# Performance work log

Hardware: AMD Instinct MI355X
Metric: run time of the kernel (lower is better)

The kernel has to match this reference:

```python
import jax, jax.numpy as jnp
import numpy as np

D_MODEL = 1024
N_HEADS = 16
D_HEAD = D_MODEL // N_HEADS
ROPE_BASE = 10000.0


def setup_inputs() -> dict:
    key = jax.random.key(0)
    k1, k2, k3, k4, k5 = jax.random.split(key, 5)
    std = 0.02 / np.sqrt(2 * 12)  # scaled_xavier with n_layers=12
    x = jax.random.normal(k1, (2, 2048, D_MODEL), dtype=jnp.float32)
    qkv_w = jax.random.normal(k2, (3 * D_MODEL, D_MODEL), dtype=jnp.float32) * std
    qkv_b = jnp.zeros((3 * D_MODEL,), dtype=jnp.float32)
    proj_w = jax.random.normal(k3, (D_MODEL, D_MODEL), dtype=jnp.float32) * std
    proj_b = jnp.zeros((D_MODEL,), dtype=jnp.float32)
    return {"x": x, "qkv_w": qkv_w, "qkv_b": qkv_b, "proj_w": proj_w, "proj_b": proj_b}


def _rope_cos_sin(seq_len, dtype):
    inv_freq = 1.0 / (ROPE_BASE ** (jnp.arange(0, D_HEAD, 2, dtype=jnp.float32) / D_HEAD))
    t = jnp.arange(seq_len, dtype=jnp.float32)
    freqs = jnp.einsum("t,d->td", t, inv_freq)          # [S, Dh/2]
    freqs = jnp.concatenate([freqs, freqs], axis=-1)      # [S, Dh]
    return jnp.cos(freqs).astype(dtype), jnp.sin(freqs).astype(dtype)


def _rotate_half(x):
    x1, x2 = jnp.split(x, 2, axis=-1)
    return jnp.concatenate([-x2, x1], axis=-1)


def reference(x, qkv_w, qkv_b, proj_w, proj_b):
    B, S, D = x.shape
    H, Dh = N_HEADS, D_HEAD
    scale = 1.0 / np.sqrt(Dh)

    qkv = x @ qkv_w.T + qkv_b                              # [B, S, 3D]
    qkv = qkv.reshape(B, S, 3, H, Dh)
    q = jnp.transpose(qkv[:, :, 0], (0, 2, 1, 3))          # [B, H, S, Dh]
    k = jnp.transpose(qkv[:, :, 1], (0, 2, 1, 3))
    v = jnp.transpose(qkv[:, :, 2], (0, 2, 1, 3))

    cos, sin = _rope_cos_sin(S, x.dtype)                   # [S, Dh]
    q = q * cos + _rotate_half(q) * sin
    k = k * cos + _rotate_half(k) * sin

    scores = jnp.einsum("bhsd,bhtd->bhst", q, k) * scale   # [B, H, S, S]
    causal = jnp.triu(jnp.ones((S, S), dtype=bool), k=1)
    neg = jnp.finfo(scores.dtype).min
    scores = jnp.where(causal[None, None], neg, scores)

    probs = jax.nn.softmax(scores, axis=-1)
    ctx = jnp.einsum("bhst,bhtd->bhsd", probs, v)          # [B, H, S, Dh]
    out = jnp.transpose(ctx, (0, 2, 1, 3)).reshape(B, S, D)
    out = out @ proj_w.T + proj_b
    return out
```

## Files before the change

### kernel.cpp

```cpp
#include <hip/hip_runtime.h>
#include <hip/hip_bf16.h>

#define BATCH 2
#define SEQ   2048
#define DMODEL 1024
#define NHEADS 16
#define DHEAD  64
#define MTOT   (BATCH * SEQ)
#define QKSTR  2048

typedef __attribute__((ext_vector_type(8))) short bf16x8;
typedef __attribute__((ext_vector_type(4))) float f32x4;

__device__ __forceinline__ void glds16(const void* g, void* l)
{
    __builtin_amdgcn_global_load_lds(
        (const __attribute__((address_space(1))) unsigned int*)g,
        (__attribute__((address_space(3))) unsigned int*)l, 16, 0, 0);
}

__global__ void cast_all_kernel(
    const float* __restrict__ a, __hip_bfloat16* __restrict__ oa, int na4,
    const float* __restrict__ b, __hip_bfloat16* __restrict__ ob, int nb4,
    const float* __restrict__ c, __hip_bfloat16* __restrict__ oc, int nc4)
{
    int i = blockIdx.x * blockDim.x + threadIdx.x;
    const float* src; __hip_bfloat16* dst; int j = i;
    if (j < na4) { src = a; dst = oa; }
    else {
        j -= na4;
        if (j < nb4) { src = b; dst = ob; }
        else {
            j -= nb4;
            if (j >= nc4) return;
            src = c; dst = oc;
        }
    }
    float4 v = ((const float4*)src)[j];
    __hip_bfloat16 tmp[4];
    tmp[0] = __float2bfloat16(v.x);
    tmp[1] = __float2bfloat16(v.y);
    tmp[2] = __float2bfloat16(v.z);
    tmp[3] = __float2bfloat16(v.w);
    *(uint2*)(dst + 4 * (size_t)j) = *(const uint2*)tmp;
}

#define GTM 64
#define GBK 64

__device__ __forceinline__ void store_out(float* p, float v) { *p = v; }
__device__ __forceinline__ void store_out(__hip_bfloat16* p, float v) { *p = __float2bfloat16(v); }

template <typename OutT, int MODE, int TN>
__global__ __launch_bounds__(256, 6) void gemm_bias_kernel(
    const __hip_bfloat16* __restrict__ A, const __hip_bfloat16* __restrict__ W,
    const float* __restrict__ bias, OutT* __restrict__ out,
    __hip_bfloat16* __restrict__ vtg,
    int M, int N, int K)
{
    const int NI = TN / 32;
    const int bm = blockIdx.x * GTM;
    const int bn = blockIdx.y * TN;
    const int tid = threadIdx.x;
    const int wave = tid >> 6;
    const int lane = tid & 63;
    const int quad = lane >> 4;
    const int l16 = lane & 15;
    const int wm = (wave & 1) * 32;
    const int wn = (wave >> 1) * (TN / 2);

    __shared__ __hip_bfloat16 As[GTM * GBK];
    __shared__ __hip_bfloat16 Bs[TN * GBK];

    f32x4 acc[2][NI] = {};

    const int srow = lane >> 3;
    const int gc8 = (((lane & 7) ^ srow)) * 8;

    for (int kt = 0; kt < K; kt += GBK) {
#pragma unroll
        for (int t = 0; t < 2; t++) {
            int i = wave * 2 + t;
            glds16(A + (size_t)(bm + i * 8 + srow) * K + kt + gc8, As + i * 512);
        }
#pragma unroll
        for (int t = 0; t < TN / 32; t++) {
            int i = wave * (TN / 32) + t;
            glds16(W + (size_t)(bn + i * 8 + srow) * K + kt + gc8, Bs + i * 512);
        }
        __syncthreads();

#pragma unroll
        for (int kk = 0; kk < 2; kk++) {
            bf16x8 af[2], bfr[NI];
#pragma unroll
            for (int i = 0; i < 2; i++) {
                int ra = wm + i * 16 + l16;
                af[i] = *(const bf16x8*)(As + ra * 64 + (((kk << 2) + quad) ^ (ra & 7)) * 8);
            }
#pragma unroll
            for (int i = 0; i < NI; i++) {
                int rb = wn + i * 16 + l16;
                bfr[i] = *(const bf16x8*)(Bs + rb * 64 + (((kk << 2) + quad) ^ (rb & 7)) * 8);
            }
#pragma unroll
            for (int mi = 0; mi < 2; mi++)
#pragma unroll
                for (int ni = 0; ni < NI; ni++)
                    acc[mi][ni] = __builtin_amdgcn_mfma_f32_16x16x32_bf16(
                        af[mi], bfr[ni], acc[mi][ni], 0, 0, 0);
        }
        __syncthreads();
    }

    if (MODE == 1 && (bn + wn) < 2 * DMODEL) {
#pragma unroll
        for (int ni = 0; ni < 2; ni++) {
            int col = bn + wn + ni * 16 + l16;
            int i32 = col & 31;
            float invf = exp2f(-13.287712379549449f * (float)i32 * (1.0f / 32.0f));
            float b1 = bias[col], b2 = bias[col + 32];
#pragma unroll
            for (int mi = 0; mi < 2; mi++) {
#pragma unroll
                for (int r = 0; r < 4; r++) {
                    int row = bm + wm + mi * 16 + quad * 4 + r;
                    int s = row & (SEQ - 1);
                    float ang = (float)s * invf;
                    float sn, cs;
                    __sincosf(ang, &sn, &cs);
                    float x1 = acc[mi][ni][r] + b1;
                    float x2 = acc[mi][ni + 2][r] + b2;
                    store_out(&out[(size_t)row * QKSTR + col], x1 * cs - x2 * sn);
                    store_out(&out[(size_t)row * QKSTR + col + 32], x2 * cs + x1 * sn);
                }
            }
        }
    } else if (MODE == 1) {
#pragma unroll
        for (int ni = 0; ni < NI; ni++) {
            int colg = bn + wn + ni * 16 + l16;
            int vcol = colg - 2 * DMODEL;
            int hh = vcol >> 6, dh = vcol & 63;
            float bv = bias[colg];
#pragma unroll
            for (int mi = 0; mi < 2; mi++) {
                int row0 = bm + wm + mi * 16 + quad * 4;
                int bb = row0 >> 11;
                int ss = row0 & (SEQ - 1);
                __hip_bfloat16 tmp[4];
#pragma unroll
                for (int r = 0; r < 4; r++)
                    tmp[r] = __float2bfloat16(acc[mi][ni][r] + bv);
                *(uint2*)(vtg + (((size_t)bb * NHEADS + hh) * DHEAD + dh) * SEQ + ss) =
                    *(uint2*)tmp;
            }
        }
    } else {
#pragma unroll
        for (int mi = 0; mi < 2; mi++)
#pragma unroll
            for (int ni = 0; ni < NI; ni++) {
                int col = bn + wn + ni * 16 + l16;
                float bv = bias[col];
#pragma unroll
                for (int r = 0; r < 4; r++) {
                    int row = bm + wm + mi * 16 + quad * 4 + r;
                    store_out(&out[(size_t)row * N + col], acc[mi][ni][r] + bv);
                }
            }
    }
}

__global__ __launch_bounds__(512, 4) void flash_attn_mfma_kernel(
    const __hip_bfloat16* __restrict__ qkb,
    const __hip_bfloat16* __restrict__ vtg,
    __hip_bfloat16* __restrict__ ctx)
{
    const int bh = blockIdx.x;
    const int b = bh >> 4, h = bh & 15;
    const int y = blockIdx.y;
    const int qa = y, qb = 31 - y;
    const int tid = threadIdx.x;
    const int w = tid >> 6;
    const int lane = tid & 63;
    const int quad = lane >> 4;
    const int l16 = lane & 15;
    const int w4 = w & 3;
    const int qt = (w >> 2) ? qb : qa;

    __shared__ __hip_bfloat16 Ks[2][64 * 64];
    __shared__ __hip_bfloat16 Vt[2][64 * 64];
    __shared__ __hip_bfloat16 Ps[128 * 64];

    const __hip_bfloat16* qbase = qkb + (size_t)b * SEQ * QKSTR + h * DHEAD;
    const __hip_bfloat16* kbase = qbase + DMODEL;
    const __hip_bfloat16* vbase = vtg + (size_t)bh * DHEAD * SEQ;

    const __hip_bfloat16* qrow = qbase + (size_t)(qt * 64 + w4 * 16 + l16) * QKSTR;
    bf16x8 qf0 = *(const bf16x8*)(qrow + quad * 8);
    bf16x8 qf1 = *(const bf16x8*)(qrow + 32 + quad * 8);

    const int srow = lane >> 3;
    const int gc8 = ((lane & 7) ^ srow) * 8;
    const __hip_bfloat16* kg = kbase + (size_t)(w * 8 + srow) * QKSTR + gc8;
    const __hip_bfloat16* vg = vbase + (size_t)(w * 8 + srow) * SEQ + gc8;

    const int xr = l16 & 7;
    const int fo0 = l16 * 64 + ((quad ^ xr) << 3);
    const int fo1 = l16 * 64 + (((4 + quad) ^ xr) << 3);
    const int pband = w * 16;
    const int pfo0 = (pband + l16) * 64 + ((quad ^ xr) << 3);
    const int pfo1 = (pband + l16) * 64 + (((4 + quad) ^ xr) << 3);

    const short onev = (l16 == 0) ? (short)0x3F80 : (short)0;
    const bf16x8 ones = {onev, onev, onev, onev, onev, onev, onev, onev};

    glds16(kg, &Ks[0][w * 512]);
    glds16(vg, &Vt[0][w * 512]);

    f32x4 oacc[5] = {};

    for (int jt = 0; jt <= qb; jt++) {
        __syncthreads();
        const int cur = jt & 1;
        if (jt < qb) {
            glds16(kg + (size_t)(jt + 1) * 64 * QKSTR, &Ks[cur ^ 1][w * 512]);
            glds16(vg + (jt + 1) * 64, &Vt[cur ^ 1][w * 512]);
        }
        if (jt <= qt) {
            const __hip_bfloat16* ks = Ks[cur];
            const __hip_bfloat16* vs = Vt[cur];

            f32x4 s4[4] = {};
#pragma unroll
            for (int nt = 0; nt < 4; nt++)
                s4[nt] = __builtin_amdgcn_mfma_f32_16x16x32_bf16(
                    qf0, *(const bf16x8*)(ks + nt * 1024 + fo0), s4[nt], 0, 0, 0);
#pragma unroll
            for (int nt = 0; nt < 4; nt++)
                s4[nt] = __builtin_amdgcn_mfma_f32_16x16x32_bf16(
                    qf1, *(const bf16x8*)(ks + nt * 1024 + fo1), s4[nt], 0, 0, 0);

            const bool diag = (jt == qt);
#pragma unroll
            for (int nt = 0; nt < 4; nt++)
#pragma unroll
                for (int r = 0; r < 4; r++) {
                    float p = __expf(s4[nt][r] * 0.125f);
                    if (diag)
                        p = (nt * 16 + l16 <= w4 * 16 + quad * 4 + r) ? p : 0.f;
                    int rr = quad * 4 + r;
                    Ps[(pband + rr) * 64 +
                       (((nt * 2 + (l16 >> 3)) ^ (rr & 7)) << 3) + xr] =
                        __float2bfloat16(p);
                }

            bf16x8 pf0 = *(const bf16x8*)(Ps + pfo0);
            bf16x8 pf1 = *(const bf16x8*)(Ps + pfo1);
#pragma unroll
            for (int dt = 0; dt < 4; dt++)
                oacc[dt] = __builtin_amdgcn_mfma_f32_16x16x32_bf16(
                    pf0, *(const bf16x8*)(vs + dt * 1024 + fo0), oacc[dt], 0, 0, 0);
            oacc[4] = __builtin_amdgcn_mfma_f32_16x16x32_bf16(pf0, ones, oacc[4], 0, 0, 0);
#pragma unroll
            for (int dt = 0; dt < 4; dt++)
                oacc[dt] = __builtin_amdgcn_mfma_f32_16x16x32_bf16(
                    pf1, *(const bf16x8*)(vs + dt * 1024 + fo1), oacc[dt], 0, 0, 0);
            oacc[4] = __builtin_amdgcn_mfma_f32_16x16x32_bf16(pf1, ones, oacc[4], 0, 0, 0);
        }
    }

#pragma unroll
    for (int r = 0; r < 4; r++) {
        float lv = __shfl(oacc[4][r], lane & 48);
        float il = 1.0f / lv;
        int qg = qt * 64 + w4 * 16 + quad * 4 + r;
        __hip_bfloat16* op = ctx + (((size_t)b * SEQ + qg) * NHEADS + h) * DHEAD + l16;
#pragma unroll
        for (int dt = 0; dt < 4; dt++)
            op[dt * 16] = __float2bfloat16(oacc[dt][r] * il);
    }
}

extern "C" void kernel_launch(void* const* d_in, const int* in_sizes, int n_in,
                              void* d_out, int out_size, void* d_ws, size_t ws_size,
                              hipStream_t stream)
{
    const float* x      = (const float*)d_in[0];
    const float* qkv_w  = (const float*)d_in[1];
    const float* qkv_b  = (const float*)d_in[2];
    const float* proj_w = (const float*)d_in[3];
    const float* proj_b = (const float*)d_in[4];
    float* out = (float*)d_out;

    char* w = (char*)d_ws;
    __hip_bfloat16* qkb = (__hip_bfloat16*)w;  w += (size_t)MTOT * QKSTR * 2;
    __hip_bfloat16* vtg = (__hip_bfloat16*)w;  w += (size_t)MTOT * DMODEL * 2;
    __hip_bfloat16* ctx = (__hip_bfloat16*)w;  w += (size_t)MTOT * DMODEL * 2;
    __hip_bfloat16* xb  = (__hip_bfloat16*)w;  w += (size_t)MTOT * DMODEL * 2;
    __hip_bfloat16* wqk = (__hip_bfloat16*)w;  w += (size_t)3 * DMODEL * DMODEL * 2;
    __hip_bfloat16* wpr = (__hip_bfloat16*)w;

    const int na4 = MTOT * DMODEL / 4;
    const int nb4 = 3 * DMODEL * DMODEL / 4;
    const int nc4 = DMODEL * DMODEL / 4;

    cast_all_kernel<<<(na4 + nb4 + nc4 + 255) / 256, 256, 0, stream>>>(
        x, xb, na4, qkv_w, wqk, nb4, proj_w, wpr, nc4);

    gemm_bias_kernel<__hip_bfloat16, 1, 128>
        <<<dim3(MTOT / GTM, (3 * DMODEL) / 128), 256, 0, stream>>>(
        xb, wqk, qkv_b, qkb, vtg, MTOT, 3 * DMODEL, DMODEL);

    flash_attn_mfma_kernel<<<dim3(BATCH * NHEADS, 16), 512, 0, stream>>>(qkb, vtg, ctx);

    gemm_bias_kernel<float, 0, 64>
        <<<dim3(MTOT / GTM, DMODEL / 64), 256, 0, stream>>>(
        ctx, wpr, proj_b, out, nullptr, MTOT, DMODEL, DMODEL);
}
```

Before: 175.1 us.

## Split long causal tile across both wave groups after short tile completes

After the short query tile finishes, the wave group that handled it now takes alternate KV tiles for the long query tile instead of idling. Partial numerator and denominator accumulators are then summed through shared memory before the output is written. K/V staging becomes a 4-slot ring that loads two tiles per iteration, and exp uses exp2 with a folded log2e scale. This raises LDS use and register pressure, which may reduce occupancy.

After: 175.3 us. About the same (+0.1%).

```diff
diff --git a/kernel.cpp b/kernel.cpp
--- a/kernel.cpp
+++ b/kernel.cpp
@@ -187,19 +187,23 @@
     const int quad = lane >> 4;
     const int l16 = lane & 15;
     const int w4 = w & 3;
-    const int qt = (w >> 2) ? qb : qa;
-
-    __shared__ __hip_bfloat16 Ks[2][64 * 64];
-    __shared__ __hip_bfloat16 Vt[2][64 * 64];
-    __shared__ __hip_bfloat16 Ps[128 * 64];
+    const int grp = w >> 2;
+    const int qtp = grp ? qb : qa;
+
+    __shared__ alignas(16) __hip_bfloat16 Ks[4][64 * 64];
+    __shared__ alignas(16) __hip_bfloat16 Vt[4][64 * 64];
+    __shared__ alignas(16) __hip_bfloat16 Ps[128 * 64];
 
     const __hip_bfloat16* qbase = qkb + (size_t)b * SEQ * QKSTR + h * DHEAD;
     const __hip_bfloat16* kbase = qbase + DMODEL;
     const __hip_bfloat16* vbase = vtg + (size_t)bh * DHEAD * SEQ;
 
-    const __hip_bfloat16* qrow = qbase + (size_t)(qt * 64 + w4 * 16 + l16) * QKSTR;
-    bf16x8 qf0 = *(const bf16x8*)(qrow + quad * 8);
-    bf16x8 qf1 = *(const bf16x8*)(qrow + 32 + quad * 8);
+    const __hip_bfloat16* qrowp = qbase + (size_t)(qtp * 64 + w4 * 16 + l16) * QKSTR;
+    bf16x8 qp0 = *(const bf16x8*)(qrowp + quad * 8);
+    bf16x8 qp1 = *(const bf16x8*)(qrowp + 32 + quad * 8);
+    const __hip_bfloat16* qrows = qbase + (size_t)(qb * 64 + w4 * 16 + l16) * QKSTR;
+    bf16x8 qs0 = *(const bf16x8*)(qrows + quad * 8);
+    bf16x8 qs1 = *(const bf16x8*)(qrows + 32 + quad * 8);
 
     const int srow = lane >> 3;
     const int gc8 = ((lane & 7) ^ srow) * 8;
@@ -216,70 +220,103 @@
     const short onev = (l16 == 0) ? (short)0x3F80 : (short)0;
     const bf16x8 ones = {onev, onev, onev, onev, onev, onev, onev, onev};
 
-    glds16(kg, &Ks[0][w * 512]);
-    glds16(vg, &Vt[0][w * 512]);
-
     f32x4 oacc[5] = {};
-
-    for (int jt = 0; jt <= qb; jt++) {
+    f32x4 oacc2[5] = {};
+
+    auto stage = [&](int t) {
+        glds16(kg + (size_t)t * 64 * QKSTR, &Ks[t & 3][w * 512]);
+        glds16(vg + t * 64, &Vt[t & 3][w * 512]);
+    };
+
+    auto compute = [&](const __hip_bfloat16* ks, const __hip_bfloat16* vs,
+                       bf16x8 f0, bf16x8 f1, f32x4* oa, bool diag) {
+        f32x4 s4[4] = {};
+#pragma unroll
+        for (int nt = 0; nt < 4; nt++)
+            s4[nt] = __builtin_amdgcn_mfma_f32_16x16x32_bf16(
+                f0, *(const bf16x8*)(ks + nt * 1024 + fo0), s4[nt], 0, 0, 0);
+#pragma unroll
+        for (int nt = 0; nt < 4; nt++)
+            s4[nt] = __builtin_amdgcn_mfma_f32_16x16x32_bf16(
+                f1, *(const bf16x8*)(ks + nt * 1024 + fo1), s4[nt], 0, 0, 0);
+
+#pragma unroll
+        for (int nt = 0; nt < 4; nt++)
+#pragma unroll
+            for (int r = 0; r < 4; r++) {
+                float p = exp2f(s4[nt][r] * 0.1803368801f);
+                if (diag)
+                    p = (nt * 16 + l16 <= w4 * 16 + quad * 4 + r) ? p : 0.f;
+                int rr = quad * 4 + r;
+                Ps[(pband + rr) * 64 +
+                   (((nt * 2 + (l16 >> 3)) ^ (rr & 7)) << 3) + xr] =
+                    __float2bfloat16(p);
+            }
+
+        bf16x8 pf0 = *(const bf16x8*)(Ps + pfo0);
+        bf16x8 pf1 = *(const bf16x8*)(Ps + pfo1);
+#pragma unroll
+        for (int dt = 0; dt < 4; dt++)
+            oa[dt] = __builtin_amdgcn_mfma_f32_16x16x32_bf16(
+                pf0, *(const bf16x8*)(vs + dt * 1024 + fo0), oa[dt], 0, 0, 0);
+        oa[4] = __builtin_amdgcn_mfma_f32_16x16x32_bf16(pf0, ones, oa[4], 0, 0, 0);
+#pragma unroll
+        for (int dt = 0; dt < 4; dt++)
+            oa[dt] = __builtin_amdgcn_mfma_f32_16x16x32_bf16(
+                pf1, *(const bf16x8*)(vs + dt * 1024 + fo1), oa[dt], 0, 0, 0);
+        oa[4] = __builtin_amdgcn_mfma_f32_16x16x32_bf16(pf1, ones, oa[4], 0, 0, 0);
+    };
+
+    stage(0);
+    const int nit = qa + 1 + ((qb - qa + 1) >> 1);
+
+    for (int n = 0; n < nit; n++) {
         __syncthreads();
-        const int cur = jt & 1;
-        if (jt < qb) {
-            glds16(kg + (size_t)(jt + 1) * 64 * QKSTR, &Ks[cur ^ 1][w * 512]);
-            glds16(vg + (jt + 1) * 64, &Vt[cur ^ 1][w * 512]);
-        }
-        if (jt <= qt) {
-            const __hip_bfloat16* ks = Ks[cur];
-            const __hip_bfloat16* vs = Vt[cur];
-
-            f32x4 s4[4] = {};
-#pragma unroll
-            for (int nt = 0; nt < 4; nt++)
-                s4[nt] = __builtin_amdgcn_mfma_f32_16x16x32_bf16(
-                    qf0, *(const bf16x8*)(ks + nt * 1024 + fo0), s4[nt], 0, 0, 0);
-#pragma unroll
-            for (int nt = 0; nt < 4; nt++)
-                s4[nt] = __builtin_amdgcn_mfma_f32_16x16x32_bf16(
-                    qf1, *(const bf16x8*)(ks + nt * 1024 + fo1), s4[nt], 0, 0, 0);
-
-            const bool diag = (jt == qt);
-#pragma unroll
-            for (int nt = 0; nt < 4; nt++)
-#pragma unroll
-                for (int r = 0; r < 4; r++) {
-                    float p = __expf(s4[nt][r] * 0.125f);
-                    if (diag)
-                        p = (nt * 16 + l16 <= w4 * 16 + quad * 4 + r) ? p : 0.f;
-                    int rr = quad * 4 + r;
-                    Ps[(pband + rr) * 64 +
-                       (((nt * 2 + (l16 >> 3)) ^ (rr & 7)) << 3) + xr] =
-                        __float2bfloat16(p);
-                }
-
-            bf16x8 pf0 = *(const bf16x8*)(Ps + pfo0);
-            bf16x8 pf1 = *(const bf16x8*)(Ps + pfo1);
+        if (n < qa) {
+            stage(n + 1);
+        } else {
+            int t0n = 2 * n - qa + 1;
+            if (t0n <= qb) stage(t0n);
+            if (t0n + 1 <= qb) stage(t0n + 1);
+        }
+        if (n <= qa) {
+            compute(&Ks[n & 3][0], &Vt[n & 3][0], qp0, qp1, oacc, n == qtp);
+        } else {
+            int t = 2 * n - qa - 1 + grp;
+            if (t <= qb) {
+                if (grp) compute(&Ks[t & 3][0], &Vt[t & 3][0], qp0, qp1, oacc, t == qb);
+                else     compute(&Ks[t & 3][0], &Vt[t & 3][0], qs0, qs1, oacc2, t == qb);
+            }
+        }
+    }
+
+    auto write_ctx = [&](f32x4* oa, int qt) {
+#pragma unroll
+        for (int r = 0; r < 4; r++) {
+            float lv = __shfl(oa[4][r], lane & 48);
+            float il = 1.0f / lv;
+            int qg = qt * 64 + w4 * 16 + quad * 4 + r;
+            __hip_bfloat16* op = ctx + (((size_t)b * SEQ + qg) * NHEADS + h) * DHEAD + l16;
 #pragma unroll
             for (int dt = 0; dt < 4; dt++)
-                oacc[dt] = __builtin_amdgcn_mfma_f32_16x16x32_bf16(
-                    pf0, *(const bf16x8*)(vs + dt * 1024 + fo0), oacc[dt], 0, 0, 0);
-            oacc[4] = __builtin_amdgcn_mfma_f32_16x16x32_bf16(pf0, ones, oacc[4], 0, 0, 0);
-#pragma unroll
-            for (int dt = 0; dt < 4; dt++)
-                oacc[dt] = __builtin_amdgcn_mfma_f32_16x16x32_bf16(
-                    pf1, *(const bf16x8*)(vs + dt * 1024 + fo1), oacc[dt], 0, 0, 0);
-            oacc[4] = __builtin_amdgcn_mfma_f32_16x16x32_bf16(pf1, ones, oacc[4], 0, 0, 0);
-        }
-    }
-
-#pragma unroll
-    for (int r = 0; r < 4; r++) {
-        float lv = __shfl(oacc[4][r], lane & 48);
-        float il = 1.0f / lv;
-        int qg = qt * 64 + w4 * 16 + quad * 4 + r;
-        __hip_bfloat16* op = ctx + (((size_t)b * SEQ + qg) * NHEADS + h) * DHEAD + l16;
-#pragma unroll
-        for (int dt = 0; dt < 4; dt++)
-            op[dt * 16] = __float2bfloat16(oacc[dt][r] * il);
+                op[dt * 16] = __float2bfloat16(oa[dt][r] * il);
+        }
+    };
+
+    __syncthreads();
+    f32x4* red = (f32x4*)&Ks[0][0];
+    if (!grp) {
+        f32x4* rp = red + ((w * 64 + lane) * 5);
+#pragma unroll
+        for (int i = 0; i < 5; i++) rp[i] = oacc2[i];
+        write_ctx(oacc, qa);
+    }
+    __syncthreads();
+    if (grp) {
+        f32x4* rp = red + (((w - 4) * 64 + lane) * 5);
+#pragma unroll
+        for (int i = 0; i < 5; i++) oacc[i] += rp[i];
+        write_ctx(oacc, qb);
     }
 }
 
```

## Split attention blocks per query tile and pack P stores via transposed MFMA

Applied to the files above, without the earlier changes.

The attention kernel moves from 512-thread blocks that paired a short and a long causal query tile to 256-thread blocks that each own one query tile. The grid doubles and is ordered so the longest tiles launch first, which removes the waves that sat idle once the short tile finished. The QK^T MFMA operands are swapped so each lane holds four consecutive keys for one query. That lets P be converted with v_cvt_pk_bf16 and written as 8-byte stores instead of scalar bf16 writes. It also switches exp to exp2 with a folded scale and adds s_setprio around the MFMA sections; the risk is a less favourable scheduling or occupancy balance on the larger grid.

New measurement: 173.8 us. No clear change (-0.7%).

```diff
diff --git a/kernel.cpp b/kernel.cpp
--- a/kernel.cpp
+++ b/kernel.cpp
@@ -17,6 +17,13 @@
     __builtin_amdgcn_global_load_lds(
         (const __attribute__((address_space(1))) unsigned int*)g,
         (__attribute__((address_space(3))) unsigned int*)l, 16, 0, 0);
+}
+
+__device__ __forceinline__ unsigned cvt_pk_bf16(float lo, float hi)
+{
+    unsigned r;
+    asm("v_cvt_pk_bf16_f32 %0, %1, %2" : "=v"(r) : "v"(lo), "v"(hi));
+    return r;
 }
 
 __global__ void cast_all_kernel(
@@ -172,110 +179,127 @@
     }
 }
 
-__global__ __launch_bounds__(512, 4) void flash_attn_mfma_kernel(
+__global__ __launch_bounds__(256, 4) void flash_attn_mfma_kernel(
     const __hip_bfloat16* __restrict__ qkb,
     const __hip_bfloat16* __restrict__ vtg,
     __hip_bfloat16* __restrict__ ctx)
 {
     const int bh = blockIdx.x;
     const int b = bh >> 4, h = bh & 15;
-    const int y = blockIdx.y;
-    const int qa = y, qb = 31 - y;
+    const int qt = 31 - blockIdx.y;
     const int tid = threadIdx.x;
     const int w = tid >> 6;
     const int lane = tid & 63;
     const int quad = lane >> 4;
     const int l16 = lane & 15;
-    const int w4 = w & 3;
-    const int qt = (w >> 2) ? qb : qa;
-
-    __shared__ __hip_bfloat16 Ks[2][64 * 64];
-    __shared__ __hip_bfloat16 Vt[2][64 * 64];
-    __shared__ __hip_bfloat16 Ps[128 * 64];
+
+    __shared__ alignas(16) __hip_bfloat16 Ks[2][64 * 64];
+    __shared__ alignas(16) __hip_bfloat16 Vt[2][64 * 64];
+    __shared__ alignas(16) __hip_bfloat16 Ps[64 * 64];
 
     const __hip_bfloat16* qbase = qkb + (size_t)b * SEQ * QKSTR + h * DHEAD;
     const __hip_bfloat16* kbase = qbase + DMODEL;
     const __hip_bfloat16* vbase = vtg + (size_t)bh * DHEAD * SEQ;
 
-    const __hip_bfloat16* qrow = qbase + (size_t)(qt * 64 + w4 * 16 + l16) * QKSTR;
+    const __hip_bfloat16* qrow = qbase + (size_t)(qt * 64 + w * 16 + l16) * QKSTR;
     bf16x8 qf0 = *(const bf16x8*)(qrow + quad * 8);
     bf16x8 qf1 = *(const bf16x8*)(qrow + 32 + quad * 8);
 
     const int srow = lane >> 3;
     const int gc8 = ((lane & 7) ^ srow) * 8;
-    const __hip_bfloat16* kg = kbase + (size_t)(w * 8 + srow) * QKSTR + gc8;
-    const __hip_bfloat16* vg = vbase + (size_t)(w * 8 + srow) * SEQ + gc8;
+    const __hip_bfloat16* kg = kbase + (size_t)(w * 16 + srow) * QKSTR + gc8;
+    const __hip_bfloat16* vg = vbase + (size_t)(w * 16 + srow) * SEQ + gc8;
 
     const int xr = l16 & 7;
     const int fo0 = l16 * 64 + ((quad ^ xr) << 3);
     const int fo1 = l16 * 64 + (((4 + quad) ^ xr) << 3);
     const int pband = w * 16;
-    const int pfo0 = (pband + l16) * 64 + ((quad ^ xr) << 3);
-    const int pfo1 = (pband + l16) * 64 + (((4 + quad) ^ xr) << 3);
+    char* const psb = (char*)Ps;
+    const int pr0 = (pband + l16) * 128 + ((quad ^ xr) << 4);
+    const int pr1 = (pband + l16) * 128 + (((4 + quad) ^ xr) << 4);
+    int pwc[4];
+#pragma unroll
+    for (int nt = 0; nt < 4; nt++)
+        pwc[nt] = (pband + l16) * 128 +
+                  ((((nt << 1) + (quad >> 1)) ^ xr) << 4) + (quad & 1) * 8;
 
     const short onev = (l16 == 0) ? (short)0x3F80 : (short)0;
     const bf16x8 ones = {onev, onev, onev, onev, onev, onev, onev, onev};
 
-    glds16(kg, &Ks[0][w * 512]);
-    glds16(vg, &Vt[0][w * 512]);
-
     f32x4 oacc[5] = {};
 
-    for (int jt = 0; jt <= qb; jt++) {
+    auto stage = [&](int t, int buf) {
+        const __hip_bfloat16* kt_ = kg + (size_t)t * 64 * QKSTR;
+        const __hip_bfloat16* vt_ = vg + t * 64;
+        glds16(kt_,              &Ks[buf][w * 1024]);
+        glds16(kt_ + 8 * QKSTR,  &Ks[buf][w * 1024 + 512]);
+        glds16(vt_,              &Vt[buf][w * 1024]);
+        glds16(vt_ + 8 * SEQ,    &Vt[buf][w * 1024 + 512]);
+    };
+
+    stage(0, 0);
+
+    for (int jt = 0; jt <= qt; jt++) {
         __syncthreads();
         const int cur = jt & 1;
-        if (jt < qb) {
-            glds16(kg + (size_t)(jt + 1) * 64 * QKSTR, &Ks[cur ^ 1][w * 512]);
-            glds16(vg + (jt + 1) * 64, &Vt[cur ^ 1][w * 512]);
-        }
-        if (jt <= qt) {
-            const __hip_bfloat16* ks = Ks[cur];
-            const __hip_bfloat16* vs = Vt[cur];
-
-            f32x4 s4[4] = {};
-#pragma unroll
-            for (int nt = 0; nt < 4; nt++)
-                s4[nt] = __builtin_amdgcn_mfma_f32_16x16x32_bf16(
-                    qf0, *(const bf16x8*)(ks + nt * 1024 + fo0), s4[nt], 0, 0, 0);
-#pragma unroll
-            for (int nt = 0; nt < 4; nt++)
-                s4[nt] = __builtin_amdgcn_mfma_f32_16x16x32_bf16(
-                    qf1, *(const bf16x8*)(ks + nt * 1024 + fo1), s4[nt], 0, 0, 0);
-
-            const bool diag = (jt == qt);
-#pragma unroll
-            for (int nt = 0; nt < 4; nt++)
-#pragma unroll
-                for (int r = 0; r < 4; r++) {
-                    float p = __expf(s4[nt][r] * 0.125f);
-                    if (diag)
-                        p = (nt * 16 + l16 <= w4 * 16 + quad * 4 + r) ? p : 0.f;
-                    int rr = quad * 4 + r;
-                    Ps[(pband + rr) * 64 +
-                       (((nt * 2 + (l16 >> 3)) ^ (rr & 7)) << 3) + xr] =
-                        __float2bfloat16(p);
-                }
-
-            bf16x8 pf0 = *(const bf16x8*)(Ps + pfo0);
-            bf16x8 pf1 = *(const bf16x8*)(Ps + pfo1);
-#pragma unroll
-            for (int dt = 0; dt < 4; dt++)
-                oacc[dt] = __builtin_amdgcn_mfma_f32_16x16x32_bf16(
-                    pf0, *(const bf16x8*)(vs + dt * 1024 + fo0), oacc[dt], 0, 0, 0);
-            oacc[4] = __builtin_amdgcn_mfma_f32_16x16x32_bf16(pf0, ones, oacc[4], 0, 0, 0);
-#pragma unroll
-            for (int dt = 0; dt < 4; dt++)
-                oacc[dt] = __builtin_amdgcn_mfma_f32_16x16x32_bf16(
-                    pf1, *(const bf16x8*)(vs + dt * 1024 + fo1), oacc[dt], 0, 0, 0);
-            oacc[4] = __builtin_amdgcn_mfma_f32_16x16x32_bf16(pf1, ones, oacc[4], 0, 0, 0);
-        }
+        if (jt < qt) stage(jt + 1, cur ^ 1);
+        const __hip_bfloat16* ks = Ks[cur];
+        const __hip_bfloat16* vs = Vt[cur];
+
+        f32x4 s4[4] = {};
+        __builtin_amdgcn_s_setprio(1);
+#pragma unroll
+        for (int nt = 0; nt < 4; nt++)
+            s4[nt] = __builtin_amdgcn_mfma_f32_16x16x32_bf16(
+                *(const bf16x8*)(ks + nt * 1024 + fo0), qf0, s4[nt], 0, 0, 0);
+#pragma unroll
+        for (int nt = 0; nt < 4; nt++)
+            s4[nt] = __builtin_amdgcn_mfma_f32_16x16x32_bf16(
+                *(const bf16x8*)(ks + nt * 1024 + fo1), qf1, s4[nt], 0, 0, 0);
+        __builtin_amdgcn_s_setprio(0);
+
+        const bool diag = (jt == qt);
+        const int qq = w * 16 + l16;
+#pragma unroll
+        for (int nt = 0; nt < 4; nt++) {
+            float p0 = exp2f(s4[nt][0] * 0.1803368801f);
+            float p1 = exp2f(s4[nt][1] * 0.1803368801f);
+            float p2 = exp2f(s4[nt][2] * 0.1803368801f);
+            float p3 = exp2f(s4[nt][3] * 0.1803368801f);
+            if (diag) {
+                int k0 = nt * 16 + quad * 4;
+                p0 = (k0 + 0 <= qq) ? p0 : 0.f;
+                p1 = (k0 + 1 <= qq) ? p1 : 0.f;
+                p2 = (k0 + 2 <= qq) ? p2 : 0.f;
+                p3 = (k0 + 3 <= qq) ? p3 : 0.f;
+            }
+            uint2 pv;
+            pv.x = cvt_pk_bf16(p0, p1);
+            pv.y = cvt_pk_bf16(p2, p3);
+            *(uint2*)(psb + pwc[nt]) = pv;
+        }
+
+        bf16x8 pf0 = *(const bf16x8*)(psb + pr0);
+        bf16x8 pf1 = *(const bf16x8*)(psb + pr1);
+        __builtin_amdgcn_s_setprio(1);
+#pragma unroll
+        for (int dt = 0; dt < 4; dt++)
+            oacc[dt] = __builtin_amdgcn_mfma_f32_16x16x32_bf16(
+                pf0, *(const bf16x8*)(vs + dt * 1024 + fo0), oacc[dt], 0, 0, 0);
+        oacc[4] = __builtin_amdgcn_mfma_f32_16x16x32_bf16(pf0, ones, oacc[4], 0, 0, 0);
+#pragma unroll
+        for (int dt = 0; dt < 4; dt++)
+            oacc[dt] = __builtin_amdgcn_mfma_f32_16x16x32_bf16(
+                pf1, *(const bf16x8*)(vs + dt * 1024 + fo1), oacc[dt], 0, 0, 0);
+        oacc[4] = __builtin_amdgcn_mfma_f32_16x16x32_bf16(pf1, ones, oacc[4], 0, 0, 0);
+        __builtin_amdgcn_s_setprio(0);
     }
 
 #pragma unroll
     for (int r = 0; r < 4; r++) {
         float lv = __shfl(oacc[4][r], lane & 48);
         float il = 1.0f / lv;
-        int qg = qt * 64 + w4 * 16 + quad * 4 + r;
+        int qg = qt * 64 + w * 16 + quad * 4 + r;
         __hip_bfloat16* op = ctx + (((size_t)b * SEQ + qg) * NHEADS + h) * DHEAD + l16;
 #pragma unroll
         for (int dt = 0; dt < 4; dt++)
@@ -313,7 +337,7 @@
         <<<dim3(MTOT / GTM, (3 * DMODEL) / 128), 256, 0, stream>>>(
         xb, wqk, qkv_b, qkb, vtg, MTOT, 3 * DMODEL, DMODEL);
 
-    flash_attn_mfma_kernel<<<dim3(BATCH * NHEADS, 16), 512, 0, stream>>>(qkb, vtg, ctx);
+    flash_attn_mfma_kernel<<<dim3(BATCH * NHEADS, 32), 256, 0, stream>>>(qkb, vtg, ctx);
 
     gemm_bias_kernel<float, 0, 64>
         <<<dim3(MTOT / GTM, DMODEL / 64), 256, 0, stream>>>(
```
